# Performance work log

Measured on AMD Instinct MI355X. Metric: run time of the kernel, lower is better.

Reference implementation:

```python
import jax, jax.numpy as jnp
import numpy as np

N_NODES = 100000


def setup_inputs() -> dict:
    key = jax.random.key(0)
    ks = jax.random.split(key, 9)
    E = 1600000
    x = jax.random.normal(ks[0], (N_NODES, 12), dtype=jnp.float32)
    edge_index = jax.random.randint(ks[1], (2, E), 0, N_NODES, dtype=jnp.int64)
    def glorot(k, shape):
        lim = float(np.sqrt(6.0 / (shape[0] + shape[1])))
        return jax.random.uniform(k, shape, jnp.float32, -lim, lim)
    return {
        "x": x,
        "edge_index": edge_index,
        "W1": glorot(ks[2], (12, 64)),
        "b1": jnp.zeros((64,), jnp.float32),
        "W2": glorot(ks[3], (64, 128)),
        "b2": jnp.zeros((128,), jnp.float32),
        "W3": glorot(ks[4], (128, 96)),
        "b3": jnp.zeros((96,), jnp.float32),
    }


def reference(x, edge_index, W1, b1, W2, b2, W3, b3):
    N = x.shape[0]
    F_channel, n_his = 8, 12
    src, dst = edge_index[0], edge_index[1]
    # add self loops (PyG GCNConv default)
    loop = jnp.arange(N, dtype=src.dtype)
    src = jnp.concatenate([src, loop])
    dst = jnp.concatenate([dst, loop])
    # symmetric normalization: norm_e = deg[src]^-1/2 * deg[dst]^-1/2
    deg = jax.ops.segment_sum(jnp.ones_like(src, dtype=x.dtype), dst, num_segments=N)
    dinv = jnp.where(deg > 0, jax.lax.rsqrt(deg), 0.0)
    norm = dinv[src] * dinv[dst]  # [E+N]

    def gcn(h, W, b):
        hw = h @ W  # transform first (out_ch <= in-edge fanout cost)
        agg = jax.ops.segment_sum(hw[src] * norm[:, None], dst, num_segments=N)
        return agg + b

    h = jax.nn.relu(gcn(x, W1, b1))
    h = jax.nn.relu(gcn(h, W2, b2))
    h = gcn(h, W3, b3)
    return h.reshape(N, F_channel, n_his)
```

## Files before the change

kernel.cpp:

```cpp
#include <hip/hip_runtime.h>
#include <hip/hip_bf16.h>
#include <hip/hip_fp16.h>


static inline int cdiv(int a, int b) { return (a + b - 1) / b; }
constexpr int BLOCK = 256;
constexpr int BSHIFT = 9;
constexpr int BNODES = 1 << BSHIFT;

typedef float nfloat4 __attribute__((ext_vector_type(4)));
typedef _Float16 hh2 __attribute__((ext_vector_type(2)));
typedef _Float16 f16x8 __attribute__((ext_vector_type(8)));
typedef float f32x16 __attribute__((ext_vector_type(16)));

#if __has_builtin(__builtin_amdgcn_fdot2)
__device__ __forceinline__ float FDOT2(hh2 a, hh2 b, float c) {
    return __builtin_amdgcn_fdot2(a, b, c, false);
}
#else
__device__ __forceinline__ float FDOT2(hh2 a, hh2 b, float c) {
    return c + (float)a.x * (float)b.x + (float)a.y * (float)b.y;
}
#endif


__global__ void zero_int_kernel(int* __restrict__ p, int n) {
    int i = blockIdx.x * blockDim.x + threadIdx.x;
    if (i < n) p[i] = 0;
}

__device__ __forceinline__ void nt_store_raw16(void* p, float4 v) {
    nfloat4 nv;
    nv.x = v.x; nv.y = v.y; nv.z = v.z; nv.w = v.w;
    __builtin_nontemporal_store(nv, (nfloat4*)p);
}

struct h4 { __half2 a, b; };
__device__ __forceinline__ void store_h4(__half* p, float4 v) {
    h4 r;
    r.a = __floats2half2_rn(v.x, v.y);
    r.b = __floats2half2_rn(v.z, v.w);
    *(h4*)p = r;
}

__device__ __forceinline__ void h8_add(float* acc, float4 raw) {
    union { float4 f; __half2 h[4]; } u;
    u.f = raw;
#pragma unroll
    for (int j = 0; j < 4; ++j) {
        float2 p = __half22float2(u.h[j]);
        acc[2 * j] += p.x;
        acc[2 * j + 1] += p.y;
    }
}


template <int CHUNK>
__global__ void bucket_count_kernel(const int* __restrict__ dst, int E,
                                    int* __restrict__ bcnt, int NB) {
    __shared__ int cnt[256];
    for (int i = threadIdx.x; i < NB; i += blockDim.x) cnt[i] = 0;
    __syncthreads();
    const int e0 = blockIdx.x * CHUNK;
    const int e1 = min(e0 + CHUNK, E);
    for (int e = e0 + threadIdx.x; e < e1; e += blockDim.x)
        atomicAdd(&cnt[dst[e] >> BSHIFT], 1);
    __syncthreads();
    for (int i = threadIdx.x; i < NB; i += blockDim.x)
        if (cnt[i]) atomicAdd(&bcnt[i], cnt[i]);
}

__global__ void bucket_scan_kernel(const int* __restrict__ bcnt, int* __restrict__ gbase,
                                   int* __restrict__ gcur, int NB) {
    __shared__ int tmp[256];
    int t = threadIdx.x;
    int v = (t < NB) ? bcnt[t] : 0;
    tmp[t] = v;
    __syncthreads();
    for (int off = 1; off < 256; off <<= 1) {
        int add = (t >= off) ? tmp[t - off] : 0;
        __syncthreads();
        tmp[t] += add;
        __syncthreads();
    }
    if (t < NB) { int ex = tmp[t] - v; gbase[t] = ex; gcur[t] = ex; }
}

template <int CHUNK>
__global__ void bin_edges_kernel(const int* __restrict__ ei, int E,
                                 int* __restrict__ gcur, unsigned* __restrict__ binned,
                                 int NB) {
    __shared__ int cnt[256], base[256], rk[256];
    for (int i = threadIdx.x; i < NB; i += blockDim.x) { cnt[i] = 0; rk[i] = 0; }
    __syncthreads();
    const int e0 = blockIdx.x * CHUNK;
    const int e1 = min(e0 + CHUNK, E);
    for (int e = e0 + threadIdx.x; e < e1; e += blockDim.x)
        atomicAdd(&cnt[ei[E + e] >> BSHIFT], 1);
    __syncthreads();
    for (int i = threadIdx.x; i < NB; i += blockDim.x)
        base[i] = atomicAdd(&gcur[i], cnt[i]);
    __syncthreads();
    for (int e = e0 + threadIdx.x; e < e1; e += blockDim.x) {
        int s = ei[e], d = ei[E + e];
        int b = d >> BSHIFT;
        int r = atomicAdd(&rk[b], 1);
        binned[base[b] + r] = (unsigned)s | ((unsigned)(d & (BNODES - 1)) << 17);
    }
}

__global__ void csr_fill_kernel(const int* __restrict__ gbase, const int* __restrict__ bcnt,
                                const unsigned* __restrict__ binned,
                                int* __restrict__ deg, float* __restrict__ dinv,
                                int* __restrict__ row_ptr, int* __restrict__ csr_src,
                                int* __restrict__ dh, int N) {
    __shared__ int c[BNODES];
    __shared__ int ps[256];
    __shared__ int dhloc[64];
    const int t = threadIdx.x;
    const int b = blockIdx.x;
    const int node0 = b << BSHIFT;
    c[t] = 0; c[t + 256] = 0;
    if (t < 64) dhloc[t] = 0;
    __syncthreads();
    const int base = gbase[b];
    const int end = base + bcnt[b];
    for (int e = base + t; e < end; e += 256)
        atomicAdd(&c[binned[e] >> 17], 1);
    __syncthreads();
    const int s0 = c[2 * t], s1 = c[2 * t + 1];
    const int pv = s0 + s1;
    ps[t] = pv;
    __syncthreads();
    for (int off = 1; off < 256; off <<= 1) {
        int add = (t >= off) ? ps[t - off] : 0;
        __syncthreads();
        ps[t] += add;
        __syncthreads();
    }
    const int ex = ps[t] - pv;
    const int p0 = base + ex;
    const int p1 = p0 + s0;
    const int n0 = node0 + 2 * t;
    if (n0 < N) {
        row_ptr[n0] = p0; deg[n0] = s0; dinv[n0] = rsqrtf((float)s0 + 1.0f);
        atomicAdd(&dhloc[min(s0, 63)], 1);
        if (n0 + 1 < N) {
            row_ptr[n0 + 1] = p1; deg[n0 + 1] = s1; dinv[n0 + 1] = rsqrtf((float)s1 + 1.0f);
            atomicAdd(&dhloc[min(s1, 63)], 1);
        }
    }
    c[2 * t] = p0; c[2 * t + 1] = p1;
    __syncthreads();
    if (t < 64 && dhloc[t]) atomicAdd(&dh[t], dhloc[t]);
    for (int e = base + t; e < end; e += 256) {
        unsigned sd = binned[e];
        int pos = atomicAdd(&c[sd >> 17], 1);
        csr_src[pos] = (int)(sd & 0x1FFFFu);
    }
}


__global__ void dscan_kernel(int* __restrict__ dh) {
    __shared__ int tmp[64];
    int t = threadIdx.x;
    int v = dh[t];
    tmp[t] = v;
    __syncthreads();
    for (int off = 1; off < 64; off <<= 1) {
        int add = (t >= off) ? tmp[t - off] : 0;
        __syncthreads();
        tmp[t] += add;
        __syncthreads();
    }
    dh[t] = tmp[t] - v;
}

__global__ void dperm_kernel(const int* __restrict__ deg, int* __restrict__ dh,
                             int* __restrict__ perm, int N) {
    __shared__ int cnt[64], base[64], rk[64];
    const int t = threadIdx.x;
    if (t < 64) { cnt[t] = 0; rk[t] = 0; }
    __syncthreads();
    const int i = blockIdx.x * blockDim.x + t;
    const int myb = (i < N) ? min(deg[i], 63) : -1;
    if (myb >= 0) atomicAdd(&cnt[myb], 1);
    __syncthreads();
    if (t < 64) base[t] = cnt[t] ? atomicAdd(&dh[t], cnt[t]) : 0;
    __syncthreads();
    if (myb >= 0) {
        int r = atomicAdd(&rk[myb], 1);
        perm[base[myb] + r] = i;
    }
}


__global__ void prescale_kernel(const float* __restrict__ x, const float* __restrict__ dinv,
                                float* __restrict__ xs, int N) {
    int t = blockIdx.x * blockDim.x + threadIdx.x;
    if (t >= N * 3) return;
    int i = t / 3;
    float di = dinv[i];
    float4 v = ((const float4*)x)[t];
    v.x *= di; v.y *= di; v.z *= di; v.w *= di;
    ((float4*)xs)[t] = v;
}


__device__ __forceinline__ void fma4(float4& acc, float s, const float4& w) {
    acc.x = fmaf(s, w.x, acc.x);
    acc.y = fmaf(s, w.y, acc.y);
    acc.z = fmaf(s, w.z, acc.z);
    acc.w = fmaf(s, w.w, acc.w);
}

__device__ __forceinline__ float4 epilogue4(float4 r, const float* bias, int c0,
                                            bool has_bias, bool relu, bool scale, float di) {
    if (has_bias) {
        const float4 bb = *(const float4*)(bias + c0);
        r.x += bb.x; r.y += bb.y; r.z += bb.z; r.w += bb.w;
    }
    if (relu) {
        r.x = fmaxf(r.x, 0.f); r.y = fmaxf(r.y, 0.f);
        r.z = fmaxf(r.z, 0.f); r.w = fmaxf(r.w, 0.f);
    }
    if (scale) { r.x *= di; r.y *= di; r.z *= di; r.w *= di; }
    return r;
}

template <int IN, int OUT, bool HAS_BIAS, bool RELU, bool SCALE, bool OUT_HALF>
__global__ void transform_kernel(const float* __restrict__ h, const float* __restrict__ W,
                                 const float* __restrict__ bias, const float* __restrict__ dinv,
                                 void* __restrict__ out_v, int N) {
    constexpr int CG = OUT / 4;
    constexpr int THREADS = 8 * CG;
    __shared__ float Ws[IN * OUT];
    for (int i = threadIdx.x; i < IN * OUT / 4; i += THREADS)
        ((float4*)Ws)[i] = ((const float4*)W)[i];
    __syncthreads();

    const int c0 = (threadIdx.x % CG) * 4;
    const int r0 = blockIdx.x * 32 + (threadIdx.x / CG) * 4;
    if (r0 >= N) return;

    const float* __restrict__ hr = h + (size_t)r0 * IN;
    float4 acc[4];
#pragma unroll
    for (int i = 0; i < 4; ++i) acc[i] = make_float4(0.f, 0.f, 0.f, 0.f);

#pragma unroll
    for (int k = 0; k < IN; k += 4) {
        float4 a[4];
#pragma unroll
        for (int i = 0; i < 4; ++i) a[i] = *(const float4*)(hr + (size_t)i * IN + k);
        const float4 w0 = *(const float4*)(Ws + (k + 0) * OUT + c0);
        const float4 w1 = *(const float4*)(Ws + (k + 1) * OUT + c0);
        const float4 w2 = *(const float4*)(Ws + (k + 2) * OUT + c0);
        const float4 w3 = *(const float4*)(Ws + (k + 3) * OUT + c0);
#pragma unroll
        for (int i = 0; i < 4; ++i) {
            fma4(acc[i], a[i].x, w0);
            fma4(acc[i], a[i].y, w1);
            fma4(acc[i], a[i].z, w2);
            fma4(acc[i], a[i].w, w3);
        }
    }

#pragma unroll
    for (int i = 0; i < 4; ++i) {
        float di = SCALE ? dinv[r0 + i] : 0.f;
        float4 r = epilogue4(acc[i], bias, c0, HAS_BIAS, RELU, SCALE, di);
        if (OUT_HALF)
            store_h4((__half*)out_v + (size_t)(r0 + i) * OUT + c0, r);
        else
            *(float4*)((float*)out_v + (size_t)(r0 + i) * OUT + c0) = r;
    }
}


__global__ void prep_w_kernel(const float* __restrict__ W2, const float* __restrict__ W3,
                              __half* __restrict__ W2T, __half* __restrict__ W3T) {
    int i = blockIdx.x * 256 + threadIdx.x;
    if (i < 64 * 128) {
        int k = i >> 7, n = i & 127;
        W2T[n * 64 + k] = __float2half(W2[i]);
    } else {
        int j = i - 64 * 128;
        if (j < 128 * 96) {
            int k = j / 96, n = j - k * 96;
            W3T[n * 128 + k] = __float2half(W3[j]);
        }
    }
}

__global__ void fused_t2t3_kernel(const __half* __restrict__ agg1,
                                  const __half* __restrict__ W2T,
                                  const float* __restrict__ b2,
                                  const __half* __restrict__ W3T,
                                  const float* __restrict__ dinv,
                                  __half* __restrict__ out,
                                  int N) {
    constexpr int LDH = 136;
    __shared__ _Float16 h2s[4][32 * LDH];
    const int lane = threadIdx.x & 63;
    const int wid = threadIdx.x >> 6;
    const int l31 = lane & 31;
    const int lh = lane >> 5;
    _Float16* hs = h2s[wid];

    float b2v[4];
#pragma unroll
    for (int nt = 0; nt < 4; ++nt) b2v[nt] = b2[nt * 32 + l31];

    const int NT = N >> 5;
    for (int t = blockIdx.x * 4 + wid; t < NT; t += gridDim.x * 4) {
        const int r0 = t << 5;

        f16x8 a2[4];
#pragma unroll
        for (int kb = 0; kb < 4; ++kb)
            a2[kb] = *(const f16x8*)(agg1 + (size_t)(r0 + l31) * 64 + kb * 16 + lh * 8);
#pragma unroll
        for (int nt = 0; nt < 4; ++nt) {
            f32x16 c = {0.f, 0.f, 0.f, 0.f, 0.f, 0.f, 0.f, 0.f,
                        0.f, 0.f, 0.f, 0.f, 0.f, 0.f, 0.f, 0.f};
#pragma unroll
            for (int kb = 0; kb < 4; ++kb) {
                f16x8 b = *(const f16x8*)(W2T + (size_t)(nt * 32 + l31) * 64 + kb * 16 + lh * 8);
                c = __builtin_amdgcn_mfma_f32_32x32x16_f16(a2[kb], b, c, 0, 0, 0);
            }
#pragma unroll
            for (int r = 0; r < 16; ++r) {
                int row = (r & 3) + 8 * (r >> 2) + 4 * lh;
                float v = fmaxf(c[r] + b2v[nt], 0.f);
                hs[row * LDH + nt * 32 + l31] = (_Float16)v;
            }
        }

        f16x8 a3[8];
#pragma unroll
        for (int kb = 0; kb < 8; ++kb)
            a3[kb] = *(const f16x8*)(hs + l31 * LDH + kb * 16 + lh * 8);
        float4 dv[4];
#pragma unroll
        for (int rg = 0; rg < 4; ++rg)
            dv[rg] = *(const float4*)(dinv + r0 + rg * 8 + lh * 4);
#pragma unroll
        for (int nt = 0; nt < 3; ++nt) {
            f32x16 c = {0.f, 0.f, 0.f, 0.f, 0.f, 0.f, 0.f, 0.f,
                        0.f, 0.f, 0.f, 0.f, 0.f, 0.f, 0.f, 0.f};
#pragma unroll
            for (int kb = 0; kb < 8; ++kb) {
                f16x8 b = *(const f16x8*)(W3T + (size_t)(nt * 32 + l31) * 128 + kb * 16 + lh * 8);
                c = __builtin_amdgcn_mfma_f32_32x32x16_f16(a3[kb], b, c, 0, 0, 0);
            }
#pragma unroll
            for (int r = 0; r < 16; ++r) {
                int row = (r & 3) + 8 * (r >> 2) + 4 * lh;
                float dvv = ((const float*)&dv[r >> 2])[r & 3];
                hs[row * LDH + nt * 32 + l31] = (_Float16)(c[r] * dvv);
            }
        }

#pragma unroll
        for (int it = 0; it < 6; ++it) {
            int id = lane + it * 64;
            int row = id / 12, ch = id - row * 12;
            float4 v = *(const float4*)(hs + row * LDH + ch * 8);
            *(float4*)((char*)(out + (size_t)r0 * 96) + (size_t)id * 16) = v;
        }
    }
}

template <int IN, int OUT, bool HAS_BIAS, bool RELU, bool SCALE, bool OUT_HALF>
__global__ void transform_h_kernel(const __half* __restrict__ h, const float* __restrict__ W,
                                   const float* __restrict__ bias, const float* __restrict__ dinv,
                                   void* __restrict__ out_v, int N) {
    constexpr int CG = OUT / 4;
    constexpr int THREADS = 8 * CG;
    __shared__ hh2 Ws[(IN / 2) * OUT];
    for (int i = threadIdx.x; i < (IN / 2) * OUT; i += THREADS) {
        int k2 = i / OUT, col = i - k2 * OUT;
        hh2 w;
        w.x = (_Float16)W[(2 * k2) * OUT + col];
        w.y = (_Float16)W[(2 * k2 + 1) * OUT + col];
        Ws[i] = w;
    }
    __syncthreads();

    const int c0 = (threadIdx.x % CG) * 4;
    const int r0 = blockIdx.x * 32 + (threadIdx.x / CG) * 4;
    if (r0 >= N) return;

    const __half* __restrict__ hr = h + (size_t)r0 * IN;
    float4 acc[4];
#pragma unroll
    for (int i = 0; i < 4; ++i) acc[i] = make_float4(0.f, 0.f, 0.f, 0.f);

#pragma unroll
    for (int k = 0; k < IN; k += 8) {
        union { float4 f; hh2 p[4]; } a[4];
#pragma unroll
        for (int r = 0; r < 4; ++r) a[r].f = *(const float4*)(hr + (size_t)r * IN + k);
#pragma unroll
        for (int j = 0; j < 4; ++j) {
            union { float4 f; hh2 p[4]; } w;
            w.f = *(const float4*)(Ws + ((k / 2 + j) * OUT + c0));
#pragma unroll
            for (int r = 0; r < 4; ++r) {
                acc[r].x = FDOT2(a[r].p[j], w.p[0], acc[r].x);
                acc[r].y = FDOT2(a[r].p[j], w.p[1], acc[r].y);
                acc[r].z = FDOT2(a[r].p[j], w.p[2], acc[r].z);
                acc[r].w = FDOT2(a[r].p[j], w.p[3], acc[r].w);
            }
        }
    }

#pragma unroll
    for (int i = 0; i < 4; ++i) {
        float di = SCALE ? dinv[r0 + i] : 0.f;
        float4 r = epilogue4(acc[i], bias, c0, HAS_BIAS, RELU, SCALE, di);
        if (OUT_HALF)
            store_h4((__half*)out_v + (size_t)(r0 + i) * OUT + c0, r);
        else
            *(float4*)((float*)out_v + (size_t)(r0 + i) * OUT + c0) = r;
    }
}


__device__ __forceinline__ void add4(float4& a, const float4& v) {
    a.x += v.x; a.y += v.y; a.z += v.z; a.w += v.w;
}

template <int F>
__global__ void gather_kernel(const int* __restrict__ row_ptr, const int* __restrict__ deg,
                              const int* __restrict__ csr_src,
                              const float* __restrict__ dinv, const float* __restrict__ hws,
                              float* __restrict__ out, int N) {
    constexpr int TPN = F / 4;
    int t = blockIdx.x * blockDim.x + threadIdx.x;
    if (t >= N * TPN) return;
    int i = t / TPN;
    int c = t - i * TPN;
    int f0 = c * 4;

    const int* __restrict__ sp = csr_src + row_ptr[i];
    int n = deg[i];
    float4 acc = *(const float4*)(hws + (size_t)i * F + f0);

    int k = 0;
    for (; k + 4 <= n; k += 4) {
        int s0 = sp[k + 0], s1 = sp[k + 1], s2 = sp[k + 2], s3 = sp[k + 3];
        const float4 v0 = *(const float4*)(hws + (size_t)s0 * F + f0);
        const float4 v1 = *(const float4*)(hws + (size_t)s1 * F + f0);
        const float4 v2 = *(const float4*)(hws + (size_t)s2 * F + f0);
        const float4 v3 = *(const float4*)(hws + (size_t)s3 * F + f0);
        add4(acc, v0); add4(acc, v1); add4(acc, v2); add4(acc, v3);
    }
    for (; k < n; ++k) {
        const float4 v = *(const float4*)(hws + (size_t)sp[k] * F + f0);
        add4(acc, v);
    }

    float di = dinv[i];
    float4 r;
    r.x = acc.x * di; r.y = acc.y * di; r.z = acc.z * di; r.w = acc.w * di;
    *(float4*)(out + (size_t)i * F + f0) = r;
}

template <int F, bool HAS_BIAS, bool OUT_HALF>
__global__ void gather_h_kernel(const int* __restrict__ row_ptr, const int* __restrict__ deg,
                                const int* __restrict__ csr_src, const int* __restrict__ perm,
                                const float* __restrict__ dinv, const __half* __restrict__ hws,
                                const float* __restrict__ b, void* __restrict__ out_v, int N) {
    constexpr int TPN = F / 8;
    int t = blockIdx.x * blockDim.x + threadIdx.x;
    if (t >= N * TPN) return;
    int slot = t / TPN;
    int c = t - slot * TPN;
    int i = perm[N - 1 - slot];
    int f0 = c * 8;

    const int* __restrict__ sp = csr_src + row_ptr[i];
    int n = deg[i];
    float acc[8];
    {
        union { float4 f; __half2 h[4]; } u;
        u.f = *(const float4*)(hws + (size_t)i * F + f0);
#pragma unroll
        for (int j = 0; j < 4; ++j) {
            float2 p = __half22float2(u.h[j]);
            acc[2 * j] = p.x; acc[2 * j + 1] = p.y;
        }
    }

    int k = 0;
    for (; k + 4 <= n; k += 4) {
        int s0 = sp[k + 0], s1 = sp[k + 1], s2 = sp[k + 2], s3 = sp[k + 3];
        float4 v0 = *(const float4*)(hws + (size_t)s0 * F + f0);
        float4 v1 = *(const float4*)(hws + (size_t)s1 * F + f0);
        float4 v2 = *(const float4*)(hws + (size_t)s2 * F + f0);
        float4 v3 = *(const float4*)(hws + (size_t)s3 * F + f0);
        h8_add(acc, v0); h8_add(acc, v1); h8_add(acc, v2); h8_add(acc, v3);
    }
    for (; k < n; ++k) {
        float4 v = *(const float4*)(hws + (size_t)sp[k] * F + f0);
        h8_add(acc, v);
    }

    float di = dinv[i];
    float4 r0, r1;
    if (HAS_BIAS) {
        const float4 bb0 = *(const float4*)(b + f0);
        const float4 bb1 = *(const float4*)(b + f0 + 4);
        r0.x = fmaf(acc[0], di, bb0.x); r0.y = fmaf(acc[1], di, bb0.y);
        r0.z = fmaf(acc[2], di, bb0.z); r0.w = fmaf(acc[3], di, bb0.w);
        r1.x = fmaf(acc[4], di, bb1.x); r1.y = fmaf(acc[5], di, bb1.y);
        r1.z = fmaf(acc[6], di, bb1.z); r1.w = fmaf(acc[7], di, bb1.w);
    } else {
        r0.x = acc[0] * di; r0.y = acc[1] * di; r0.z = acc[2] * di; r0.w = acc[3] * di;
        r1.x = acc[4] * di; r1.y = acc[5] * di; r1.z = acc[6] * di; r1.w = acc[7] * di;
    }
    if (OUT_HALF) {
        union { float4 f; __half2 h[4]; } u;
        u.h[0] = __floats2half2_rn(r0.x, r0.y);
        u.h[1] = __floats2half2_rn(r0.z, r0.w);
        u.h[2] = __floats2half2_rn(r1.x, r1.y);
        u.h[3] = __floats2half2_rn(r1.z, r1.w);
        nt_store_raw16((__half*)out_v + (size_t)i * F + f0, u.f);
    } else {
        float* op = (float*)out_v + (size_t)i * F + f0;
        nt_store_raw16(op, r0);
        nt_store_raw16(op + 4, r1);
    }
}


extern "C" void kernel_launch(void* const* d_in, const int* in_sizes, int n_in,
                              void* d_out, int out_size, void* d_ws, size_t ws_size,
                              hipStream_t stream) {
    const float* x  = (const float*)d_in[0];
    const int*   ei = (const int*)d_in[1];
    const float* W1 = (const float*)d_in[2];
    const float* b1 = (const float*)d_in[3];
    const float* W2 = (const float*)d_in[4];
    const float* b2 = (const float*)d_in[5];
    const float* W3 = (const float*)d_in[6];
    const float* b3 = (const float*)d_in[7];
    float* out = (float*)d_out;

    const int N = in_sizes[0] / 12;
    const int E = in_sizes[1] / 2;
    const int NB = cdiv(N, BNODES);

    char* ws = (char*)d_ws;
    int*   deg     = (int*)ws;    ws += (size_t)N * sizeof(int);
    int*   row_ptr = (int*)ws;    ws += (size_t)N * sizeof(int);
    int*   perm    = (int*)ws;    ws += (size_t)N * sizeof(int);
    int*   bcnt    = (int*)ws;    ws += 256 * sizeof(int);
    int*   dh      = (int*)ws;    ws += 64 * sizeof(int);
    int*   gbase   = (int*)ws;    ws += 256 * sizeof(int);
    int*   gcur    = (int*)ws;    ws += 256 * sizeof(int);
    float* dinv    = (float*)ws;  ws += (size_t)N * sizeof(float);
    __half* W2Th   = (__half*)ws; ws += 128 * 64 * sizeof(__half);
    __half* W3Th   = (__half*)ws; ws += 96 * 128 * sizeof(__half);
    int*   csr_src = (int*)ws;    ws += (size_t)E * sizeof(int);
    float* bufA    = (float*)ws;  ws += (size_t)N * 128 * sizeof(float);
    float* bufB    = (float*)ws;
    unsigned* binned = (unsigned*)bufB;

    zero_int_kernel<<<2, 256, 0, stream>>>(bcnt, 256 + 64);
    prep_w_kernel<<<80, 256, 0, stream>>>(W2, W3, W2Th, W3Th);
    bucket_count_kernel<4096><<<cdiv(E, 4096), BLOCK, 0, stream>>>(ei + E, E, bcnt, NB);
    bucket_scan_kernel<<<1, 256, 0, stream>>>(bcnt, gbase, gcur, NB);
    bin_edges_kernel<4096><<<cdiv(E, 4096), BLOCK, 0, stream>>>(ei, E, gcur, binned, NB);
    csr_fill_kernel<<<NB, 256, 0, stream>>>(gbase, bcnt, binned, deg, dinv, row_ptr,
                                            csr_src, dh, N);

    dscan_kernel<<<1, 64, 0, stream>>>(dh);
    dperm_kernel<<<cdiv(N, BLOCK), BLOCK, 0, stream>>>(deg, dh, perm, N);

    const int tb = cdiv(N, 32);

    prescale_kernel<<<cdiv(N * 3, BLOCK), BLOCK, 0, stream>>>(x, dinv, bufA, N);
    gather_kernel<12><<<cdiv(N * 3, BLOCK), BLOCK, 0, stream>>>(
        row_ptr, deg, csr_src, dinv, bufA, bufB, N);
    transform_kernel<12, 64, true, true, true, true><<<tb, 8 * (64 / 4), 0, stream>>>(
        bufB, W1, b1, dinv, bufA, N);

    gather_h_kernel<64, false, true><<<cdiv(N * 8, BLOCK), BLOCK, 0, stream>>>(
        row_ptr, deg, csr_src, perm, dinv, (const __half*)bufA, nullptr, bufB, N);

    fused_t2t3_kernel<<<cdiv(N / 32, 8), 256, 0, stream>>>(
        (const __half*)bufB, W2Th, b2, W3Th, dinv, (__half*)bufA, N);

    gather_h_kernel<96, true, false><<<cdiv(N * 12, BLOCK), BLOCK, 0, stream>>>(
        row_ptr, deg, csr_src, perm, dinv, (const __half*)bufA, b3, out, N);
}
```

Baseline: 328.1 us.

## Gather layer-1 input in fp16 padded rows, degree-sorted, with deeper index prefetch

The prescale kernel now writes the degree-scaled input as fp16 rows padded to 16 halves. The first-layer gather then runs two threads per node instead of three, visits nodes in degree-sorted order via perm, and reads half the bytes per neighbour. Both gather kernels gain an 8-wide unrolled loop that prefetches the next 8 neighbour indices, to increase memory-level parallelism. The risks are lower input precision, more registers per thread, and some wasted bandwidth on the padding. The unused transform_h kernel is also removed.

```diff
diff --git a/kernel.cpp b/kernel.cpp
--- a/kernel.cpp
+++ b/kernel.cpp
@@ -9,19 +9,8 @@
 constexpr int BNODES = 1 << BSHIFT;
 
 typedef float nfloat4 __attribute__((ext_vector_type(4)));
-typedef _Float16 hh2 __attribute__((ext_vector_type(2)));
 typedef _Float16 f16x8 __attribute__((ext_vector_type(8)));
 typedef float f32x16 __attribute__((ext_vector_type(16)));
-
-#if __has_builtin(__builtin_amdgcn_fdot2)
-__device__ __forceinline__ float FDOT2(hh2 a, hh2 b, float c) {
-    return __builtin_amdgcn_fdot2(a, b, c, false);
-}
-#else
-__device__ __forceinline__ float FDOT2(hh2 a, hh2 b, float c) {
-    return c + (float)a.x * (float)b.x + (float)a.y * (float)b.y;
-}
-#endif
 
 
 __global__ void zero_int_kernel(int* __restrict__ p, int n) {
@@ -195,15 +184,25 @@
 }
 
 
-__global__ void prescale_kernel(const float* __restrict__ x, const float* __restrict__ dinv,
-                                float* __restrict__ xs, int N) {
-    int t = blockIdx.x * blockDim.x + threadIdx.x;
-    if (t >= N * 3) return;
-    int i = t / 3;
+__global__ void prescale_h_kernel(const float* __restrict__ x, const float* __restrict__ dinv,
+                                  __half* __restrict__ xs, int N) {
+    int i = blockIdx.x * blockDim.x + threadIdx.x;
+    if (i >= N) return;
     float di = dinv[i];
-    float4 v = ((const float4*)x)[t];
-    v.x *= di; v.y *= di; v.z *= di; v.w *= di;
-    ((float4*)xs)[t] = v;
+    const float4* xr = (const float4*)(x + (size_t)i * 12);
+    float4 a = xr[0], b = xr[1], c = xr[2];
+    union { float4 f; __half2 h[4]; } u0, u1;
+    u0.h[0] = __floats2half2_rn(a.x * di, a.y * di);
+    u0.h[1] = __floats2half2_rn(a.z * di, a.w * di);
+    u0.h[2] = __floats2half2_rn(b.x * di, b.y * di);
+    u0.h[3] = __floats2half2_rn(b.z * di, b.w * di);
+    u1.h[0] = __floats2half2_rn(c.x * di, c.y * di);
+    u1.h[1] = __floats2half2_rn(c.z * di, c.w * di);
+    u1.h[2] = __floats2half2_rn(0.f, 0.f);
+    u1.h[3] = __floats2half2_rn(0.f, 0.f);
+    float4* op = (float4*)(xs + (size_t)i * 16);
+    op[0] = u0.f;
+    op[1] = u1.f;
 }
 
 
@@ -372,100 +371,80 @@
     }
 }
 
-template <int IN, int OUT, bool HAS_BIAS, bool RELU, bool SCALE, bool OUT_HALF>
-__global__ void transform_h_kernel(const __half* __restrict__ h, const float* __restrict__ W,
-                                   const float* __restrict__ bias, const float* __restrict__ dinv,
-                                   void* __restrict__ out_v, int N) {
-    constexpr int CG = OUT / 4;
-    constexpr int THREADS = 8 * CG;
-    __shared__ hh2 Ws[(IN / 2) * OUT];
-    for (int i = threadIdx.x; i < (IN / 2) * OUT; i += THREADS) {
-        int k2 = i / OUT, col = i - k2 * OUT;
-        hh2 w;
-        w.x = (_Float16)W[(2 * k2) * OUT + col];
-        w.y = (_Float16)W[(2 * k2 + 1) * OUT + col];
-        Ws[i] = w;
-    }
-    __syncthreads();
-
-    const int c0 = (threadIdx.x % CG) * 4;
-    const int r0 = blockIdx.x * 32 + (threadIdx.x / CG) * 4;
-    if (r0 >= N) return;
-
-    const __half* __restrict__ hr = h + (size_t)r0 * IN;
-    float4 acc[4];
-#pragma unroll
-    for (int i = 0; i < 4; ++i) acc[i] = make_float4(0.f, 0.f, 0.f, 0.f);
-
-#pragma unroll
-    for (int k = 0; k < IN; k += 8) {
-        union { float4 f; hh2 p[4]; } a[4];
-#pragma unroll
-        for (int r = 0; r < 4; ++r) a[r].f = *(const float4*)(hr + (size_t)r * IN + k);
-#pragma unroll
-        for (int j = 0; j < 4; ++j) {
-            union { float4 f; hh2 p[4]; } w;
-            w.f = *(const float4*)(Ws + ((k / 2 + j) * OUT + c0));
-#pragma unroll
-            for (int r = 0; r < 4; ++r) {
-                acc[r].x = FDOT2(a[r].p[j], w.p[0], acc[r].x);
-                acc[r].y = FDOT2(a[r].p[j], w.p[1], acc[r].y);
-                acc[r].z = FDOT2(a[r].p[j], w.p[2], acc[r].z);
-                acc[r].w = FDOT2(a[r].p[j], w.p[3], acc[r].w);
-            }
-        }
-    }
-
-#pragma unroll
-    for (int i = 0; i < 4; ++i) {
-        float di = SCALE ? dinv[r0 + i] : 0.f;
-        float4 r = epilogue4(acc[i], bias, c0, HAS_BIAS, RELU, SCALE, di);
-        if (OUT_HALF)
-            store_h4((__half*)out_v + (size_t)(r0 + i) * OUT + c0, r);
-        else
-            *(float4*)((float*)out_v + (size_t)(r0 + i) * OUT + c0) = r;
-    }
-}
-
-
-__device__ __forceinline__ void add4(float4& a, const float4& v) {
-    a.x += v.x; a.y += v.y; a.z += v.z; a.w += v.w;
-}
-
-template <int F>
-__global__ void gather_kernel(const int* __restrict__ row_ptr, const int* __restrict__ deg,
-                              const int* __restrict__ csr_src,
-                              const float* __restrict__ dinv, const float* __restrict__ hws,
-                              float* __restrict__ out, int N) {
-    constexpr int TPN = F / 4;
+
+__global__ void gather_x_kernel(const int* __restrict__ row_ptr, const int* __restrict__ deg,
+                                const int* __restrict__ csr_src, const int* __restrict__ perm,
+                                const float* __restrict__ dinv, const __half* __restrict__ xs,
+                                float* __restrict__ out, int N) {
     int t = blockIdx.x * blockDim.x + threadIdx.x;
-    if (t >= N * TPN) return;
-    int i = t / TPN;
-    int c = t - i * TPN;
-    int f0 = c * 4;
+    if (t >= N * 2) return;
+    int slot = t >> 1;
+    int c = t & 1;
+    int i = perm[N - 1 - slot];
+    int f0 = c * 8;
 
     const int* __restrict__ sp = csr_src + row_ptr[i];
     int n = deg[i];
-    float4 acc = *(const float4*)(hws + (size_t)i * F + f0);
+    float acc[8];
+    {
+        union { float4 f; __half2 h[4]; } u;
+        u.f = *(const float4*)(xs + (size_t)i * 16 + f0);
+#pragma unroll
+        for (int j = 0; j < 4; ++j) {
+            float2 p = __half22float2(u.h[j]);
+            acc[2 * j] = p.x; acc[2 * j + 1] = p.y;
+        }
+    }
 
     int k = 0;
+    if (n >= 8) {
+        int s[8];
+#pragma unroll
+        for (int j = 0; j < 8; ++j) s[j] = sp[j];
+        for (; k + 16 <= n; k += 8) {
+            int ns[8];
+#pragma unroll
+            for (int j = 0; j < 8; ++j) ns[j] = sp[k + 8 + j];
+            float4 v[8];
+#pragma unroll
+            for (int j = 0; j < 8; ++j) v[j] = *(const float4*)(xs + (size_t)s[j] * 16 + f0);
+#pragma unroll
+            for (int j = 0; j < 8; ++j) h8_add(acc, v[j]);
+#pragma unroll
+            for (int j = 0; j < 8; ++j) s[j] = ns[j];
+        }
+        float4 v[8];
+#pragma unroll
+        for (int j = 0; j < 8; ++j) v[j] = *(const float4*)(xs + (size_t)s[j] * 16 + f0);
+#pragma unroll
+        for (int j = 0; j < 8; ++j) h8_add(acc, v[j]);
+        k += 8;
+    }
     for (; k + 4 <= n; k += 4) {
         int s0 = sp[k + 0], s1 = sp[k + 1], s2 = sp[k + 2], s3 = sp[k + 3];
-        const float4 v0 = *(const float4*)(hws + (size_t)s0 * F + f0);
-        const float4 v1 = *(const float4*)(hws + (size_t)s1 * F + f0);
-        const float4 v2 = *(const float4*)(hws + (size_t)s2 * F + f0);
-        const float4 v3 = *(const float4*)(hws + (size_t)s3 * F + f0);
-        add4(acc, v0); add4(acc, v1); add4(acc, v2); add4(acc, v3);
+        float4 v0 = *(const float4*)(xs + (size_t)s0 * 16 + f0);
+        float4 v1 = *(const float4*)(xs + (size_t)s1 * 16 + f0);
+        float4 v2 = *(const float4*)(xs + (size_t)s2 * 16 + f0);
+        float4 v3 = *(const float4*)(xs + (size_t)s3 * 16 + f0);
+        h8_add(acc, v0); h8_add(acc, v1); h8_add(acc, v2); h8_add(acc, v3);
     }
     for (; k < n; ++k) {
-        const float4 v = *(const float4*)(hws + (size_t)sp[k] * F + f0);
-        add4(acc, v);
+        float4 v = *(const float4*)(xs + (size_t)sp[k] * 16 + f0);
+        h8_add(acc, v);
     }
 
     float di = dinv[i];
-    float4 r;
-    r.x = acc.x * di; r.y = acc.y * di; r.z = acc.z * di; r.w = acc.w * di;
-    *(float4*)(out + (size_t)i * F + f0) = r;
+    float* op = out + (size_t)i * 12;
+    float4 r0;
+    r0.x = acc[0] * di; r0.y = acc[1] * di; r0.z = acc[2] * di; r0.w = acc[3] * di;
+    if (c == 0) {
+        float4 r1;
+        r1.x = acc[4] * di; r1.y = acc[5] * di; r1.z = acc[6] * di; r1.w = acc[7] * di;
+        *(float4*)op = r0;
+        *(float4*)(op + 4) = r1;
+    } else {
+        *(float4*)(op + 8) = r0;
+    }
 }
 
 template <int F, bool HAS_BIAS, bool OUT_HALF>
@@ -495,6 +474,29 @@
     }
 
     int k = 0;
+    if (n >= 8) {
+        int s[8];
+#pragma unroll
+        for (int j = 0; j < 8; ++j) s[j] = sp[j];
+        for (; k + 16 <= n; k += 8) {
+            int ns[8];
+#pragma unroll
+            for (int j = 0; j < 8; ++j) ns[j] = sp[k + 8 + j];
+            float4 v[8];
+#pragma unroll
+            for (int j = 0; j < 8; ++j) v[j] = *(const float4*)(hws + (size_t)s[j] * F + f0);
+#pragma unroll
+            for (int j = 0; j < 8; ++j) h8_add(acc, v[j]);
+#pragma unroll
+            for (int j = 0; j < 8; ++j) s[j] = ns[j];
+        }
+        float4 v[8];
+#pragma unroll
+        for (int j = 0; j < 8; ++j) v[j] = *(const float4*)(hws + (size_t)s[j] * F + f0);
+#pragma unroll
+        for (int j = 0; j < 8; ++j) h8_add(acc, v[j]);
+        k += 8;
+    }
     for (; k + 4 <= n; k += 4) {
         int s0 = sp[k + 0], s1 = sp[k + 1], s2 = sp[k + 2], s3 = sp[k + 3];
         float4 v0 = *(const float4*)(hws + (size_t)s0 * F + f0);
@@ -582,9 +584,9 @@
 
     const int tb = cdiv(N, 32);
 
-    prescale_kernel<<<cdiv(N * 3, BLOCK), BLOCK, 0, stream>>>(x, dinv, bufA, N);
-    gather_kernel<12><<<cdiv(N * 3, BLOCK), BLOCK, 0, stream>>>(
-        row_ptr, deg, csr_src, dinv, bufA, bufB, N);
+    prescale_h_kernel<<<cdiv(N, BLOCK), BLOCK, 0, stream>>>(x, dinv, (__half*)bufA, N);
+    gather_x_kernel<<<cdiv(N * 2, BLOCK), BLOCK, 0, stream>>>(
+        row_ptr, deg, csr_src, perm, dinv, (const __half*)bufA, bufB, N);
     transform_kernel<12, 64, true, true, true, true><<<tb, 8 * (64 / 4), 0, stream>>>(
         bufB, W1, b1, dinv, bufA, N);
 
```

Result: no change. 330.5 us (+0.7%).
